# Performance work log

Hardware: AMD Instinct MI355X
Metric: run time of the kernel (lower is better)

Reference implementation:

```python
import jax, jax.numpy as jnp
import numpy as np

B, S, D, H = 4, 1024, 1024, 16
HD = D // H


def setup_inputs() -> dict:
    key = jax.random.key(0)
    ks = jax.random.split(key, 8)
    x = jax.random.normal(ks[0], (B, S, D), dtype=jnp.float32)
    attn_bias = jax.random.normal(ks[1], (B, H, S, S), dtype=jnp.float32) * 0.1
    pos_ids = jnp.broadcast_to(jnp.arange(S, dtype=jnp.int32), (B, S))
    lengths = jnp.array([S, S - 64, S - 128, S - 256], dtype=jnp.int32)
    pad_mask = jnp.arange(S)[None, :] >= lengths[:, None]  # True = padded key
    scale = 0.02
    Wq = jax.random.normal(ks[2], (D, D), dtype=jnp.float32) * scale
    Wk = jax.random.normal(ks[3], (D, D), dtype=jnp.float32) * scale
    Wv = jax.random.normal(ks[4], (D, D), dtype=jnp.float32) * scale
    Wo = jax.random.normal(ks[5], (D, D), dtype=jnp.float32) * scale
    bq = jnp.zeros((D,), jnp.float32); bk = jnp.zeros((D,), jnp.float32)
    bv = jnp.zeros((D,), jnp.float32); bo = jnp.zeros((D,), jnp.float32)
    return {"x": x, "attn_bias": attn_bias, "pos_ids": pos_ids, "pad_mask": pad_mask,
            "Wq": Wq, "bq": bq, "Wk": Wk, "bk": bk, "Wv": Wv, "bv": bv, "Wo": Wo, "bo": bo}


def _apply_rotary(q, k, pos_ids):
    # q,k: [B,S,H,HD]; pos_ids: [B,S]
    hd = q.shape[-1]
    inv_freq = 1.0 / (10000.0 ** (jnp.arange(0, hd, 2, dtype=jnp.float32) / hd))
    freqs = pos_ids.astype(jnp.float32)[:, :, None] * inv_freq  # [B,S,HD/2]
    emb = jnp.concatenate([freqs, freqs], axis=-1)[:, :, None, :]  # [B,S,1,HD]
    cos, sin = jnp.cos(emb), jnp.sin(emb)
    def rot_half(t):
        t1, t2 = jnp.split(t, 2, axis=-1)
        return jnp.concatenate([-t2, t1], axis=-1)
    return q * cos + rot_half(q) * sin, k * cos + rot_half(k) * sin


def reference(x, attn_bias, pos_ids, pad_mask, Wq, bq, Wk, bk, Wv, bv, Wo, bo):
    b, s, d = x.shape
    q = (x @ Wq.T + bq).reshape(b, s, H, HD)
    k = (x @ Wk.T + bk).reshape(b, s, H, HD)
    v = (x @ Wv.T + bv).reshape(b, s, H, HD)
    q, k = _apply_rotary(q, k, pos_ids)
    q = q.transpose(0, 2, 1, 3)  # [B,H,S,HD]
    k = k.transpose(0, 2, 1, 3)
    v = v.transpose(0, 2, 1, 3)
    scores = jnp.einsum("bhqd,bhkd->bhqk", q, k) / np.sqrt(HD).astype(np.float32)
    scores = scores + attn_bias
    scores = jnp.where(pad_mask[:, None, None, :], -jnp.inf, scores)
    attn = jax.nn.softmax(scores, axis=-1)  # dropout p=0 -> identity
    out = jnp.einsum("bhqk,bhkd->bqhd", attn, v).reshape(b, s, d)
    metric = k.mean(axis=1)  # mean over heads -> [B,S,HD]
    return out @ Wo.T + bo, metric
```

## Files before the change

### kernel.cpp

```cpp
#include <hip/hip_runtime.h>
#include <hip/hip_bf16.h>

#define SS 1024
#define DD 1024
#define HH 16
#define HDD 64

using f32x4  = __attribute__((ext_vector_type(4))) float;
using bf16x8 = __attribute__((ext_vector_type(8))) __bf16;
using bf16x4 = __attribute__((ext_vector_type(4))) __bf16;

__device__ __forceinline__ void gload_lds16(const void* g, void* l) {
  __builtin_amdgcn_global_load_lds((__attribute__((address_space(1))) void*)g,
                                   (__attribute__((address_space(3))) void*)l, 16, 0, 0);
}

__global__ void convert_kernel(const float4* __restrict__ x, const float4* __restrict__ Wq,
                               const float4* __restrict__ Wk, const float4* __restrict__ Wv,
                               const float4* __restrict__ Wo,
                               bf16x4* __restrict__ xb, bf16x4* __restrict__ wqkvb,
                               bf16x4* __restrict__ wob, float4* __restrict__ metric) {
  int i = blockIdx.x * 256 + threadIdx.x;
  if (blockIdx.x < 256) {
    float4 z = {0.f, 0.f, 0.f, 0.f};
    metric[blockIdx.x * 256 + threadIdx.x] = z;
  }
  float4 v; bf16x4* dst;
  if (i < 1048576)      { v = x[i];              dst = xb + i; }
  else if (i < 1310720) { v = Wq[i - 1048576];   dst = wqkvb + (i - 1048576); }
  else if (i < 1572864) { v = Wk[i - 1310720];   dst = wqkvb + 262144 + (i - 1310720); }
  else if (i < 1835008) { v = Wv[i - 1572864];   dst = wqkvb + 524288 + (i - 1572864); }
  else                  { v = Wo[i - 1835008];   dst = wob + (i - 1835008); }
  bf16x4 o;
  o[0] = (__bf16)v.x; o[1] = (__bf16)v.y; o[2] = (__bf16)v.z; o[3] = (__bf16)v.w;
  *dst = o;
}

#define GEMM_STAGE(BUF, KK)                                                        \
  {                                                                                \
    char* Ab = smem + (BUF) * 32768;                                               \
    char* Bb = Ab + 16384;                                                         \
    _Pragma("unroll") for (int q = 0; q < 4; ++q) {                                \
      int idx = q * 256 + tid;                                                     \
      int row = idx >> 3, c = idx & 7;                                             \
      gload_lds16(A  + (size_t)(m0 + row) * 1024 + (KK) + ((c ^ (row & 7)) << 3),  \
                  Ab + q * 4096 + wid * 1024);                                     \
      gload_lds16(Bm + (size_t)(n0 + row) * 1024 + (KK) + ((c ^ (row & 7)) << 3),  \
                  Bb + q * 4096 + wid * 1024);                                     \
    }                                                                              \
  }

template<int EPI>
__global__ __launch_bounds__(256, 2)
void gemm_kernel(const __bf16* __restrict__ A, const __bf16* __restrict__ Bm, int N,
                 const float* __restrict__ b0, const float* __restrict__ b1,
                 const float* __restrict__ b2, const int* __restrict__ pos_ids,
                 __bf16* __restrict__ Qr, __bf16* __restrict__ Kr, __bf16* __restrict__ Vtg,
                 float* __restrict__ metric, float* __restrict__ Cout) {
  __shared__ __align__(16) char smem[65536];
  const int tid = threadIdx.x;
  const int wid = tid >> 6, lane = tid & 63;
  const int g = lane >> 4, cl = lane & 15;
  const int ntn = N >> 7;
  const int tile = (blockIdx.x & 7) * ((int)gridDim.x >> 3) + (blockIdx.x >> 3);
  const int bm = tile / ntn, bn = tile % ntn;
  const int m0 = bm << 7, n0 = bn << 7;
  const int wr = (wid >> 1) << 6, wc = (wid & 1) << 6;
  const int swz = cl & 7;

  f32x4 acc[4][4] = {};

  GEMM_STAGE(0, 0);
  __syncthreads();
  int buf = 0;
  for (int t = 0; t < 16; ++t) {
    if (t + 1 < 16) GEMM_STAGE(buf ^ 1, (t + 1) * 64);
    const __bf16* Abuf = (const __bf16*)(smem + buf * 32768);
    const __bf16* Bbuf = Abuf + 8192;
#pragma unroll
    for (int s = 0; s < 2; ++s) {
      bf16x8 fa[4], fb[4];
#pragma unroll
      for (int i = 0; i < 4; ++i)
        fa[i] = *(const bf16x8*)(Abuf + (wr + i * 16 + cl) * 64 + (((s * 4 + g) ^ swz) << 3));
#pragma unroll
      for (int j = 0; j < 4; ++j)
        fb[j] = *(const bf16x8*)(Bbuf + (wc + j * 16 + cl) * 64 + (((s * 4 + g) ^ swz) << 3));
#pragma unroll
      for (int i = 0; i < 4; ++i)
#pragma unroll
        for (int j = 0; j < 4; ++j)
          acc[i][j] = __builtin_amdgcn_mfma_f32_16x16x32_bf16(fa[i], fb[j], acc[i][j], 0, 0, 0);
    }
    __syncthreads();
    buf ^= 1;
  }

  if constexpr (EPI == 1) {
#pragma unroll
    for (int j = 0; j < 4; ++j) {
      int col = n0 + wc + j * 16 + cl;
      float bv = b0[col];
#pragma unroll
      for (int i = 0; i < 4; ++i)
#pragma unroll
        for (int r = 0; r < 4; ++r) {
          int row = m0 + wr + i * 16 + g * 4 + r;
          Cout[(size_t)row * 1024 + col] = acc[i][j][r] + bv;
        }
    }
  } else if (n0 >= 2048) {
    __bf16* vt_s = (__bf16*)smem;
    const int b_ = m0 >> 10, s0 = m0 & 1023;
    const int vbase = n0 - 2048;
#pragma unroll
    for (int phase = 0; phase < 2; ++phase) {
      __syncthreads();
      if ((wid & 1) == phase) {
#pragma unroll
        for (int j = 0; j < 4; ++j) {
          int d = j * 16 + cl;
          float bv = b2[vbase + wc + d];
#pragma unroll
          for (int i = 0; i < 4; ++i)
#pragma unroll
            for (int r = 0; r < 4; ++r)
              vt_s[d * 136 + wr + i * 16 + g * 4 + r] = (__bf16)(acc[i][j][r] + bv);
        }
      }
      __syncthreads();
      int hh = (vbase >> 6) + phase;
#pragma unroll
      for (int p = 0; p < 4; ++p) {
        int d = p * 16 + (tid >> 4), s8 = (tid & 15) * 8;
        bf16x8 v = *(const bf16x8*)(vt_s + d * 136 + s8);
        *(bf16x8*)(Vtg + ((size_t)(b_ * HH + hh) * HDD + d) * SS + s0 + s8) = v;
      }
    }
  } else {
    const int cb = n0 + wc;
    const int region = cb >> 10;
    const int hcol = (cb & 1023) >> 6;
    const int cir = cb & 1023;
    const float* bias = region == 0 ? b0 : b1;
    __bf16* dst = region == 0 ? Qr : Kr;
    float invf0 = exp2f(-0.4152410118609203f * (float)(cl));
    float invf1 = exp2f(-0.4152410118609203f * (float)(16 + cl));
#pragma unroll
    for (int i = 0; i < 4; ++i) {
#pragma unroll
      for (int r = 0; r < 4; ++r) {
        int row = m0 + wr + i * 16 + g * 4 + r;
        int b_ = row >> 10, s = row & 1023;
        size_t ob = ((size_t)(b_ * HH + hcol) * SS + s) * HDD;
        float pos = (float)pos_ids[row];
#pragma unroll
        for (int j = 0; j < 2; ++j) {
          int dlo = j * 16 + cl;
          float vlo = acc[i][j][r]     + bias[cir + dlo];
          float vhi = acc[i][j + 2][r] + bias[cir + dlo + 32];
          float th = pos * (j == 0 ? invf0 : invf1);
          float sn, cs;
          __sincosf(th, &sn, &cs);
          float olo = vlo * cs - vhi * sn;
          float ohi = vhi * cs + vlo * sn;
          dst[ob + dlo]      = (__bf16)olo;
          dst[ob + dlo + 32] = (__bf16)ohi;
          if (region == 1) {
            atomicAdd(&metric[(size_t)row * HDD + dlo],      olo * 0.0625f);
            atomicAdd(&metric[(size_t)row * HDD + dlo + 32], ohi * 0.0625f);
          }
        }
      }
    }
  }
}

#define TILE_BODY(T, BUF, BCUR, BNXT)                                              \
  {                                                                                \
    __syncthreads();                        \
    if ((T) + 1 < ntile) {                                                         \
      const int kk = ((T) + 1) * 64;                                               \
      gload_lds16(Kb + (size_t)(kk + krow) * 64 + kchk * 8,                        \
                  (char*)&Ks[(BUF) ^ 1][8 * wid][0]);                              \
      gload_lds16(Vb + (size_t)krow * SS + kk + kchk * 8,                          \
                  (char*)&Vt[(BUF) ^ 1][8 * wid][0]);                              \
      _Pragma("unroll") for (int kt = 0; kt < 4; ++kt)                             \
        BNXT[kt] = *(const f32x4*)(Bb + (size_t)(q0 + cl) * SS + kk + kt * 16 + 4 * g); \
    }                                                                              \
    f32x4 sc[4];                                                                   \
    __builtin_amdgcn_s_setprio(1);                                                 \
    _Pragma("unroll") for (int kt = 0; kt < 4; ++kt) {                             \
      bf16x8 kb0 = *(const bf16x8*)(&Ks[(BUF)][kt * 16 + cl][(g ^ swz) * 8]);      \
      bf16x8 kb1 = *(const bf16x8*)(&Ks[(BUF)][kt * 16 + cl][((g + 4) ^ swz) * 8]);\
      f32x4 z = {0.f, 0.f, 0.f, 0.f};                                              \
      z = __builtin_amdgcn_mfma_f32_16x16x32_bf16(kb0, aq0, z, 0, 0, 0);           \
      sc[kt] = __builtin_amdgcn_mfma_f32_16x16x32_bf16(kb1, aq1, z, 0, 0, 0);      \
    }                                                                              \
    __builtin_amdgcn_s_setprio(0);                                                 \
    _Pragma("unroll") for (int kt = 0; kt < 4; ++kt)                               \
      _Pragma("unroll") for (int r = 0; r < 4; ++r)                                \
        sc[kt][r] = sc[kt][r] * 0.125f + BCUR[kt][r];                              \
    float mx = fmaxf(fmaxf(fmaxf(sc[0][0], sc[0][1]), fmaxf(sc[0][2], sc[0][3])),  \
                     fmaxf(fmaxf(sc[1][0], sc[1][1]), fmaxf(sc[1][2], sc[1][3]))); \
    mx = fmaxf(mx, fmaxf(fmaxf(fmaxf(sc[2][0], sc[2][1]), fmaxf(sc[2][2], sc[2][3])), \
                         fmaxf(fmaxf(sc[3][0], sc[3][1]), fmaxf(sc[3][2], sc[3][3])))); \
    mx = fmaxf(mx, __shfl_xor(mx, 16, 64));                                        \
    mx = fmaxf(mx, __shfl_xor(mx, 32, 64));                                        \
    if (!__all(mx <= m_l + 8.0f)) {                                                \
      float nm = fmaxf(m_l, mx);                                                   \
      float s_ = __expf(m_l - nm);                                                 \
      m_l = nm; l_l *= s_;                                                         \
      float sb0 = __shfl(s_, 4 * g + 0, 64), sb1 = __shfl(s_, 4 * g + 1, 64);      \
      float sb2 = __shfl(s_, 4 * g + 2, 64), sb3 = __shfl(s_, 4 * g + 3, 64);      \
      _Pragma("unroll") for (int dj = 0; dj < 4; ++dj) {                           \
        o[dj][0] *= sb0; o[dj][1] *= sb1; o[dj][2] *= sb2; o[dj][3] *= sb3;        \
      }                                                                            \
    }                                                                              \
    _Pragma("unroll") for (int kt = 0; kt < 4; ++kt)                               \
      _Pragma("unroll") for (int r = 0; r < 4; ++r)                                \
        sc[kt][r] = __expf(sc[kt][r] - m_l);                                       \
    float rs = ((sc[0][0] + sc[0][1]) + (sc[0][2] + sc[0][3]))                     \
             + ((sc[1][0] + sc[1][1]) + (sc[1][2] + sc[1][3]))                     \
             + ((sc[2][0] + sc[2][1]) + (sc[2][2] + sc[2][3]))                     \
             + ((sc[3][0] + sc[3][1]) + (sc[3][2] + sc[3][3]));                    \
    rs += __shfl_xor(rs, 16, 64);                                                  \
    rs += __shfl_xor(rs, 32, 64);                                                  \
    l_l += rs;                                                                     \
    _Pragma("unroll") for (int kt = 0; kt < 4; ++kt) {                             \
      bf16x4 pk;                                                                   \
      pk[0] = (__bf16)sc[kt][0]; pk[1] = (__bf16)sc[kt][1];                        \
      pk[2] = (__bf16)sc[kt][2]; pk[3] = (__bf16)sc[kt][3];                        \
      *(bf16x4*)(&Plds[wid][cl][kt * 16 + 4 * g]) = pk;                            \
    }                                                                              \
    bf16x8 pa0 = *(const bf16x8*)(&Plds[wid][cl][g * 8]);                          \
    bf16x8 pa1 = *(const bf16x8*)(&Plds[wid][cl][32 + g * 8]);                     \
    __builtin_amdgcn_s_setprio(1);                                                 \
    _Pragma("unroll") for (int dj = 0; dj < 4; ++dj) {                             \
      bf16x8 vb0 = *(const bf16x8*)(&Vt[(BUF)][dj * 16 + cl][(g ^ swz) * 8]);      \
      bf16x8 vb1 = *(const bf16x8*)(&Vt[(BUF)][dj * 16 + cl][((g + 4) ^ swz) * 8]);\
      o[dj] = __builtin_amdgcn_mfma_f32_16x16x32_bf16(pa0, vb0, o[dj], 0, 0, 0);   \
      o[dj] = __builtin_amdgcn_mfma_f32_16x16x32_bf16(pa1, vb1, o[dj], 0, 0, 0);   \
    }                                                                              \
    __builtin_amdgcn_s_setprio(0);                                                 \
  }

__global__ __launch_bounds__(512, 4)
void attn_kernel(const __bf16* __restrict__ Qr, const __bf16* __restrict__ Kr,
                 const __bf16* __restrict__ Vtg, const float* __restrict__ bias,
                 const int* __restrict__ pad, __bf16* __restrict__ attn_out) {
  __shared__ __align__(16) __bf16 Ks[2][64][64];
  __shared__ __align__(16) __bf16 Vt[2][64][64];
  __shared__ __align__(16) __bf16 Plds[8][16][72];
  const int tid = threadIdx.x;
  const int wid = tid >> 6, lane = tid & 63;
  const int g = lane >> 4, cl = lane & 15;
  const int bh = blockIdx.x & 63, b_ = bh >> 4, h = bh & 15;
  const int q0 = (blockIdx.x >> 6) * 128 + wid * 16;
  const __bf16* Qb = Qr  + ((size_t)bh << 16);
  const __bf16* Kb = Kr  + ((size_t)bh << 16);
  const __bf16* Vb = Vtg + ((size_t)bh << 16);
  const float*  Bb = bias + ((size_t)bh << 20);
  const int* padb = pad + b_ * SS;

  int pm = (lane < 16) ? padb[lane * 64] : 1;
  unsigned long long ball = __ballot(pm == 0);
  const int ntile = __popcll(ball & 0xFFFFull);

  const int l8 = lane >> 3, l7 = lane & 7;
  const int krow = 8 * wid + l8;
  const int kchk = l7 ^ l8;
  const int swz = cl & 7;

  bf16x8 aq0 = *(const bf16x8*)(Qb + (size_t)(q0 + cl) * 64 + g * 8);
  bf16x8 aq1 = *(const bf16x8*)(Qb + (size_t)(q0 + cl) * 64 + 32 + g * 8);

  gload_lds16(Kb + (size_t)krow * 64 + kchk * 8, (char*)&Ks[0][8 * wid][0]);
  gload_lds16(Vb + (size_t)krow * SS + kchk * 8, (char*)&Vt[0][8 * wid][0]);
  f32x4 bregA[4], bregB[4];
#pragma unroll
  for (int kt = 0; kt < 4; ++kt)
    bregA[kt] = *(const f32x4*)(Bb + (size_t)(q0 + cl) * SS + kt * 16 + 4 * g);

  f32x4 o[4] = {};
  float m_l = -1e30f, l_l = 0.f;

  for (int t = 0; t < ntile; t += 2) {
    TILE_BODY(t, 0, bregA, bregB);
    if (t + 1 < ntile) TILE_BODY(t + 1, 1, bregB, bregA);
  }

  float lb0 = __shfl(l_l, 4 * g + 0, 64), lb1 = __shfl(l_l, 4 * g + 1, 64);
  float lb2 = __shfl(l_l, 4 * g + 2, 64), lb3 = __shfl(l_l, 4 * g + 3, 64);
  float ib0 = 1.f / lb0, ib1 = 1.f / lb1, ib2 = 1.f / lb2, ib3 = 1.f / lb3;
#pragma unroll
  for (int dj = 0; dj < 4; ++dj) {
    int col = h * 64 + dj * 16 + cl;
    attn_out[(size_t)(b_ * SS + q0 + g * 4 + 0) * DD + col] = (__bf16)(o[dj][0] * ib0);
    attn_out[(size_t)(b_ * SS + q0 + g * 4 + 1) * DD + col] = (__bf16)(o[dj][1] * ib1);
    attn_out[(size_t)(b_ * SS + q0 + g * 4 + 2) * DD + col] = (__bf16)(o[dj][2] * ib2);
    attn_out[(size_t)(b_ * SS + q0 + g * 4 + 3) * DD + col] = (__bf16)(o[dj][3] * ib3);
  }
}

extern "C" void kernel_launch(void* const* d_in, const int* in_sizes, int n_in,
                              void* d_out, int out_size, void* d_ws, size_t ws_size,
                              hipStream_t stream) {
  const float* x  = (const float*)d_in[0];
  const float* ab = (const float*)d_in[1];
  const int* pos  = (const int*)d_in[2];
  const int* pad  = (const int*)d_in[3];
  const float* Wq = (const float*)d_in[4];
  const float* bq = (const float*)d_in[5];
  const float* Wk = (const float*)d_in[6];
  const float* bk = (const float*)d_in[7];
  const float* Wv = (const float*)d_in[8];
  const float* bv = (const float*)d_in[9];
  const float* Wo = (const float*)d_in[10];
  const float* bo = (const float*)d_in[11];
  float* out = (float*)d_out;
  float* metric = out + 4194304;

  char* ws = (char*)d_ws;
  __bf16* Qr   = (__bf16*)(ws);
  __bf16* Kr   = (__bf16*)(ws + 8388608);
  __bf16* Vtg  = (__bf16*)(ws + 16777216);
  __bf16* xb   = (__bf16*)(ws + 25165824);
  __bf16* wqkv = (__bf16*)(ws + 33554432);
  __bf16* wob  = (__bf16*)(ws + 39845888);
  __bf16* ao   = (__bf16*)(ws + 41943040);

  convert_kernel<<<8192, 256, 0, stream>>>((const float4*)x, (const float4*)Wq,
                                           (const float4*)Wk, (const float4*)Wv,
                                           (const float4*)Wo, (bf16x4*)xb,
                                           (bf16x4*)wqkv, (bf16x4*)wob, (float4*)metric);
  gemm_kernel<0><<<768, 256, 0, stream>>>(xb, wqkv, 3072, bq, bk, bv, pos,
                                          Qr, Kr, Vtg, metric, nullptr);
  attn_kernel<<<512, 512, 0, stream>>>(Qr, Kr, Vtg, ab, pad, ao);
  gemm_kernel<1><<<256, 256, 0, stream>>>(ao, wob, 1024, bo, nullptr, nullptr, nullptr,
                                          nullptr, nullptr, nullptr, nullptr, out);
}
```

Measured before the change: 158.7 us.

## Widen attention key tile to 128 with half-tile processing and smaller P buffer

The attention kernel now stages 128 keys per iteration (K and V tiles doubled in LDS) instead of 64, halving the number of block-wide barriers and loop iterations. Each 128-key tile is processed as two 64-key halves, and the P·V product is split into 32-key chunks so the per-wave P scratch shrinks to 16x40. A tail flag skips the second half when the valid key count is an odd number of 64-blocks. Trade-offs: more LDS per block, which may cut occupancy at 4 blocks/CU, and bias for the next tile is loaded after compute rather than overlapped, which weakens latency hiding.

```diff
diff --git a/kernel.cpp b/kernel.cpp
--- a/kernel.cpp
+++ b/kernel.cpp
@@ -176,23 +176,14 @@
   }
 }
 
-#define TILE_BODY(T, BUF, BCUR, BNXT)                                              \
+#define ATTN_HALF(KT0, W0, BCUR)                                                   \
   {                                                                                \
-    __syncthreads();                        \
-    if ((T) + 1 < ntile) {                                                         \
-      const int kk = ((T) + 1) * 64;                                               \
-      gload_lds16(Kb + (size_t)(kk + krow) * 64 + kchk * 8,                        \
-                  (char*)&Ks[(BUF) ^ 1][8 * wid][0]);                              \
-      gload_lds16(Vb + (size_t)krow * SS + kk + kchk * 8,                          \
-                  (char*)&Vt[(BUF) ^ 1][8 * wid][0]);                              \
-      _Pragma("unroll") for (int kt = 0; kt < 4; ++kt)                             \
-        BNXT[kt] = *(const f32x4*)(Bb + (size_t)(q0 + cl) * SS + kk + kt * 16 + 4 * g); \
-    }                                                                              \
     f32x4 sc[4];                                                                   \
     __builtin_amdgcn_s_setprio(1);                                                 \
     _Pragma("unroll") for (int kt = 0; kt < 4; ++kt) {                             \
-      bf16x8 kb0 = *(const bf16x8*)(&Ks[(BUF)][kt * 16 + cl][(g ^ swz) * 8]);      \
-      bf16x8 kb1 = *(const bf16x8*)(&Ks[(BUF)][kt * 16 + cl][((g + 4) ^ swz) * 8]);\
+      int row = (KT0 + kt) * 16 + cl;                                              \
+      bf16x8 kb0 = *(const bf16x8*)(&Ks[buf][row][(g ^ swz) * 8]);                 \
+      bf16x8 kb1 = *(const bf16x8*)(&Ks[buf][row][((g + 4) ^ swz) * 8]);           \
       f32x4 z = {0.f, 0.f, 0.f, 0.f};                                              \
       z = __builtin_amdgcn_mfma_f32_16x16x32_bf16(kb0, aq0, z, 0, 0, 0);           \
       sc[kt] = __builtin_amdgcn_mfma_f32_16x16x32_bf16(kb1, aq1, z, 0, 0, 0);      \
@@ -200,7 +191,7 @@
     __builtin_amdgcn_s_setprio(0);                                                 \
     _Pragma("unroll") for (int kt = 0; kt < 4; ++kt)                               \
       _Pragma("unroll") for (int r = 0; r < 4; ++r)                                \
-        sc[kt][r] = sc[kt][r] * 0.125f + BCUR[kt][r];                              \
+        sc[kt][r] = sc[kt][r] * 0.125f + BCUR[KT0 + kt][r];                        \
     float mx = fmaxf(fmaxf(fmaxf(sc[0][0], sc[0][1]), fmaxf(sc[0][2], sc[0][3])),  \
                      fmaxf(fmaxf(sc[1][0], sc[1][1]), fmaxf(sc[1][2], sc[1][3]))); \
     mx = fmaxf(mx, fmaxf(fmaxf(fmaxf(sc[2][0], sc[2][1]), fmaxf(sc[2][2], sc[2][3])), \
@@ -227,31 +218,40 @@
     rs += __shfl_xor(rs, 16, 64);                                                  \
     rs += __shfl_xor(rs, 32, 64);                                                  \
     l_l += rs;                                                                     \
-    _Pragma("unroll") for (int kt = 0; kt < 4; ++kt) {                             \
-      bf16x4 pk;                                                                   \
-      pk[0] = (__bf16)sc[kt][0]; pk[1] = (__bf16)sc[kt][1];                        \
-      pk[2] = (__bf16)sc[kt][2]; pk[3] = (__bf16)sc[kt][3];                        \
-      *(bf16x4*)(&Plds[wid][cl][kt * 16 + 4 * g]) = pk;                            \
+    _Pragma("unroll") for (int w = 0; w < 2; ++w) {                                \
+      _Pragma("unroll") for (int k2 = 0; k2 < 2; ++k2) {                           \
+        int kt = w * 2 + k2;                                                       \
+        bf16x4 pk;                                                                 \
+        pk[0] = (__bf16)sc[kt][0]; pk[1] = (__bf16)sc[kt][1];                      \
+        pk[2] = (__bf16)sc[kt][2]; pk[3] = (__bf16)sc[kt][3];                      \
+        *(bf16x4*)(Pw + cl * 40 + k2 * 16 + 4 * g) = pk;                           \
+      }                                                                            \
+      bf16x8 pa = *(const bf16x8*)(Pw + cl * 40 + g * 8);                          \
+      __builtin_amdgcn_s_setprio(1);                                               \
+      _Pragma("unroll") for (int dj = 0; dj < 4; ++dj) {                           \
+        int vrow = dj * 16 + cl;                                                   \
+        bf16x8 vb = *(const bf16x8*)(&Vt[buf][vrow][((((W0 + w) * 4) + g) ^ swz) * 8]); \
+        o[dj] = __builtin_amdgcn_mfma_f32_16x16x32_bf16(pa, vb, o[dj], 0, 0, 0);   \
+      }                                                                            \
+      __builtin_amdgcn_s_setprio(0);                                               \
     }                                                                              \
-    bf16x8 pa0 = *(const bf16x8*)(&Plds[wid][cl][g * 8]);                          \
-    bf16x8 pa1 = *(const bf16x8*)(&Plds[wid][cl][32 + g * 8]);                     \
-    __builtin_amdgcn_s_setprio(1);                                                 \
-    _Pragma("unroll") for (int dj = 0; dj < 4; ++dj) {                             \
-      bf16x8 vb0 = *(const bf16x8*)(&Vt[(BUF)][dj * 16 + cl][(g ^ swz) * 8]);      \
-      bf16x8 vb1 = *(const bf16x8*)(&Vt[(BUF)][dj * 16 + cl][((g + 4) ^ swz) * 8]);\
-      o[dj] = __builtin_amdgcn_mfma_f32_16x16x32_bf16(pa0, vb0, o[dj], 0, 0, 0);   \
-      o[dj] = __builtin_amdgcn_mfma_f32_16x16x32_bf16(pa1, vb1, o[dj], 0, 0, 0);   \
-    }                                                                              \
-    __builtin_amdgcn_s_setprio(0);                                                 \
+  }
+
+#define ATTN_STAGE(NB, KK)                                                         \
+  _Pragma("unroll") for (int s = 0; s < 2; ++s) {                                  \
+    gload_lds16(Kb + (size_t)((KK) + s * 64 + krow) * 64 + kchk * 8,               \
+                (char*)&Ks[NB][s * 64 + 8 * wid][0]);                              \
+    gload_lds16(Vb + (size_t)(s * 32 + vrow) * SS + (KK) + vchk * 8,               \
+                (char*)&Vt[NB][s * 32 + 4 * wid][0]);                              \
   }
 
 __global__ __launch_bounds__(512, 4)
 void attn_kernel(const __bf16* __restrict__ Qr, const __bf16* __restrict__ Kr,
                  const __bf16* __restrict__ Vtg, const float* __restrict__ bias,
                  const int* __restrict__ pad, __bf16* __restrict__ attn_out) {
-  __shared__ __align__(16) __bf16 Ks[2][64][64];
-  __shared__ __align__(16) __bf16 Vt[2][64][64];
-  __shared__ __align__(16) __bf16 Plds[8][16][72];
+  __shared__ __align__(16) __bf16 Ks[2][128][64];
+  __shared__ __align__(16) __bf16 Vt[2][64][128];
+  __shared__ __align__(16) __bf16 Plds[8][16][40];
   const int tid = threadIdx.x;
   const int wid = tid >> 6, lane = tid & 63;
   const int g = lane >> 4, cl = lane & 15;
@@ -265,29 +265,44 @@
 
   int pm = (lane < 16) ? padb[lane * 64] : 1;
   unsigned long long ball = __ballot(pm == 0);
-  const int ntile = __popcll(ball & 0xFFFFull);
-
-  const int l8 = lane >> 3, l7 = lane & 7;
-  const int krow = 8 * wid + l8;
-  const int kchk = l7 ^ l8;
+  const int valid64 = __popcll(ball & 0xFFFFull);
+  const int nt = (valid64 + 1) >> 1;
+  const int tail = valid64 & 1;
+
+  const int krow = 8 * wid + (lane >> 3);
+  const int kchk = (lane & 7) ^ (lane >> 3);
+  const int vrow = 4 * wid + (lane >> 4);
+  const int vchk = (lane & 15) ^ (vrow & 7);
   const int swz = cl & 7;
+  __bf16* Pw = &Plds[wid][0][0];
 
   bf16x8 aq0 = *(const bf16x8*)(Qb + (size_t)(q0 + cl) * 64 + g * 8);
   bf16x8 aq1 = *(const bf16x8*)(Qb + (size_t)(q0 + cl) * 64 + 32 + g * 8);
 
-  gload_lds16(Kb + (size_t)krow * 64 + kchk * 8, (char*)&Ks[0][8 * wid][0]);
-  gload_lds16(Vb + (size_t)krow * SS + kchk * 8, (char*)&Vt[0][8 * wid][0]);
-  f32x4 bregA[4], bregB[4];
-#pragma unroll
-  for (int kt = 0; kt < 4; ++kt)
-    bregA[kt] = *(const f32x4*)(Bb + (size_t)(q0 + cl) * SS + kt * 16 + 4 * g);
+  ATTN_STAGE(0, 0);
+  f32x4 breg[8];
+#pragma unroll
+  for (int kt = 0; kt < 8; ++kt)
+    breg[kt] = *(const f32x4*)(Bb + (size_t)(q0 + cl) * SS + kt * 16 + 4 * g);
 
   f32x4 o[4] = {};
   float m_l = -1e30f, l_l = 0.f;
 
-  for (int t = 0; t < ntile; t += 2) {
-    TILE_BODY(t, 0, bregA, bregB);
-    if (t + 1 < ntile) TILE_BODY(t + 1, 1, bregB, bregA);
+  for (int t = 0; t < nt; ++t) {
+    const int buf = t & 1;
+    __syncthreads();
+    if (t + 1 < nt) ATTN_STAGE(buf ^ 1, (t + 1) * 128);
+
+    ATTN_HALF(0, 0, breg);
+    if (!(tail && t == nt - 1))
+      ATTN_HALF(4, 2, breg);
+
+    if (t + 1 < nt) {
+      int kk2 = (t + 1) * 128;
+#pragma unroll
+      for (int kt = 0; kt < 8; ++kt)
+        breg[kt] = *(const f32x4*)(Bb + (size_t)(q0 + cl) * SS + kk2 + kt * 16 + 4 * g);
+    }
   }
 
   float lb0 = __shfl(l_l, 4 * g + 0, 64), lb1 = __shfl(l_l, 4 * g + 1, 64);
```

Measured after the change: 155.3 us. 2.1% less time.
